# Kernel optimization log

Hardware: AMD Instinct MI355X
Metric: run time of the kernel (lower is better)

The kernel has to match this reference:

```python
import jax, jax.numpy as jnp
import numpy as np

B, T, D = 4, 4096, 1024
LN_EPS = 1e-5

def _xavier(key, shape, gain=1.0):
    fan_in, fan_out = shape[1], shape[0]
    a = gain * np.sqrt(6.0 / (fan_in + fan_out))
    return jax.random.uniform(key, shape, jnp.float32, -a, a)

def setup_inputs() -> dict:
    key = jax.random.key(0)
    kx, kg, kv, ko = jax.random.split(key, 4)
    # log_decay param init so that softplus(log_decay) == decay_init (0.01)
    log_decay = jnp.asarray(np.log(np.expm1(0.01)), jnp.float32)
    return {
        "x": jax.random.normal(kx, (B, T, D), jnp.float32),
        "ln_w": jnp.ones((D,), jnp.float32),
        "ln_b": jnp.zeros((D,), jnp.float32),
        "gate_w": _xavier(kg, (D, D)),            # torch Linear weight [out, in]
        "gate_b": jnp.zeros((D,), jnp.float32),
        "value_w": _xavier(kv, (D, D), gain=0.01),
        "value_b": jnp.zeros((D,), jnp.float32),
        "out_w": _xavier(ko, (D, D), gain=0.01),
        "out_b": jnp.zeros((D,), jnp.float32),
        "log_decay": log_decay,
    }

def reference(x, ln_w, ln_b, gate_w, gate_b, value_w, value_b, out_w, out_b, log_decay):
    # LayerNorm over last dim
    mu = jnp.mean(x, axis=-1, keepdims=True)
    var = jnp.mean(jnp.square(x - mu), axis=-1, keepdims=True)
    normed = (x - mu) * jax.lax.rsqrt(var + LN_EPS) * ln_w + ln_b
    # gate / value projections (torch Linear: y = x @ W.T + b)
    g = jax.nn.sigmoid(normed @ gate_w.T + gate_b)
    v = normed @ value_w.T + value_b
    # push-pull: cumsum(g*v) - cumsum((1-g)*v) == cumsum((2g-1)*v)
    cumsum = jnp.cumsum((2.0 * g - 1.0) * v, axis=1)
    alpha = jax.nn.softplus(log_decay)
    positions = jnp.arange(T, dtype=jnp.float32)
    decay = jnp.exp(-alpha * positions)[None, :, None]  # [1, T, 1]
    output = cumsum * decay
    return x + (output @ out_w.T + out_b)
```

## Files before the change

### kernel.cpp

```cpp
#include <hip/hip_runtime.h>
#include <hip/hip_bf16.h>

#define BB 4
#define TT 4096
#define DD 1024
#define MM (BB * TT)
#define LN_EPS 1e-5f

typedef __attribute__((ext_vector_type(8))) short bf16x8;
typedef __attribute__((ext_vector_type(4))) float f32x4;

__device__ __forceinline__ float bfbits2f(unsigned short h) {
    return __uint_as_float(((unsigned int)h) << 16);
}
__device__ __forceinline__ unsigned short f2bfbits(float f) {
    __hip_bfloat16 h = __float2bfloat16(f);
    return *reinterpret_cast<unsigned short*>(&h);
}
__device__ __forceinline__ unsigned int pack2(float a, float b) {
    return (unsigned int)f2bfbits(a) | ((unsigned int)f2bfbits(b) << 16);
}

__device__ __forceinline__ void async_copy16(void* lds, const void* g) {
    __builtin_amdgcn_global_load_lds(
        (const __attribute__((address_space(1))) void*)g,
        (__attribute__((address_space(3))) void*)lds,
        16, 0, 0);
}

__global__ __launch_bounds__(256)
void convert_w3(const float* __restrict__ s0, const float* __restrict__ s1,
                const float* __restrict__ s2,
                __hip_bfloat16* __restrict__ d0, __hip_bfloat16* __restrict__ d1,
                __hip_bfloat16* __restrict__ d2)
{
    const int blk = blockIdx.x;
    const int w = blk >> 10;
    const float* src = (w == 0) ? s0 : (w == 1) ? s1 : s2;
    __hip_bfloat16* dst = (w == 0) ? d0 : (w == 1) ? d1 : d2;
    const size_t i = ((size_t)(blk & 1023) * 256 + threadIdx.x) * 4;
    float4 v = *(const float4*)(src + i);
    uint2 o;
    o.x = pack2(v.x, v.y);
    o.y = pack2(v.z, v.w);
    *(uint2*)((unsigned short*)dst + i) = o;
}

__global__ __launch_bounds__(256)
void ln_kernel(const float* __restrict__ x,
               const float* __restrict__ w,
               const float* __restrict__ b,
               __hip_bfloat16* __restrict__ out)
{
    const int wv   = threadIdx.x >> 6;
    const int lane = threadIdx.x & 63;
    const int row  = blockIdx.x * 4 + wv;

    const float* xr = x + (size_t)row * DD + lane * 16;
    float4 v[4];
    #pragma unroll
    for (int i = 0; i < 4; ++i) v[i] = *(const float4*)(xr + i * 4);

    float s = 0.0f, ss = 0.0f;
    #pragma unroll
    for (int i = 0; i < 4; ++i) {
        s  += (v[i].x + v[i].y) + (v[i].z + v[i].w);
        ss += fmaf(v[i].x, v[i].x, fmaf(v[i].y, v[i].y,
              fmaf(v[i].z, v[i].z, v[i].w * v[i].w)));
    }
    #pragma unroll
    for (int o = 32; o > 0; o >>= 1) {
        s  += __shfl_down(s, o);
        ss += __shfl_down(ss, o);
    }
    s  = __shfl(s, 0);
    ss = __shfl(ss, 0);

    const float mu   = s * (1.0f / DD);
    const float var  = ss * (1.0f / DD) - mu * mu;
    const float rstd = rsqrtf(var + LN_EPS);

    unsigned int res[8];
    #pragma unroll
    for (int i = 0; i < 4; ++i) {
        float4 wr = *(const float4*)(w + lane * 16 + i * 4);
        float4 br = *(const float4*)(b + lane * 16 + i * 4);
        float o0 = (v[i].x - mu) * rstd * wr.x + br.x;
        float o1 = (v[i].y - mu) * rstd * wr.y + br.y;
        float o2 = (v[i].z - mu) * rstd * wr.z + br.z;
        float o3 = (v[i].w - mu) * rstd * wr.w + br.w;
        res[i * 2]     = pack2(o0, o1);
        res[i * 2 + 1] = pack2(o2, o3);
    }
    unsigned short* op = (unsigned short*)out + (size_t)row * DD + lane * 16;
    *(uint4*)op       = make_uint4(res[0], res[1], res[2], res[3]);
    *(uint4*)(op + 8) = make_uint4(res[4], res[5], res[6], res[7]);
}

__global__ __launch_bounds__(256, 2)
void dual_gemm_gate(const __hip_bfloat16* __restrict__ A,
                    const __hip_bfloat16* __restrict__ Wg,
                    const __hip_bfloat16* __restrict__ Wv,
                    const float* __restrict__ gb,
                    const float* __restrict__ vb,
                    __hip_bfloat16* __restrict__ U,
                    int M, int N, int K)
{
    constexpr int BK = 64;
    __shared__ short As[128 * BK];
    __shared__ short Bg[128 * BK];
    __shared__ short Bv[128 * BK];

    const int tid  = threadIdx.x;
    const int m0   = blockIdx.x * 128;
    const int n0   = blockIdx.y * 128;
    const int wave = tid >> 6;
    const int lane = tid & 63;
    const int wm   = (wave & 1) * 64;
    const int wn   = (wave >> 1) * 64;
    const int lrow = lane & 15;
    const int kgrp = lane >> 4;
    const int swz  = lrow & 7;

    f32x4 accg[4][4] = {};
    f32x4 accv[4][4] = {};

    const __hip_bfloat16* gA[4];
    const __hip_bfloat16* gG[4];
    const __hip_bfloat16* gV[4];
    #pragma unroll
    for (int r = 0; r < 4; ++r) {
        const int slot = r * 256 + tid;
        const int srow = slot >> 3;
        const int gcc  = (slot & 7) ^ (srow & 7);
        gA[r] = A  + (size_t)(m0 + srow) * K + gcc * 8;
        gG[r] = Wg + (size_t)(n0 + srow) * K + gcc * 8;
        gV[r] = Wv + (size_t)(n0 + srow) * K + gcc * 8;
    }

    for (int k0 = 0; k0 < K; k0 += BK) {
        #pragma unroll
        for (int r = 0; r < 4; ++r) {
            async_copy16(&As[(r * 256 + tid) * 8], gA[r] + k0);
            async_copy16(&Bg[(r * 256 + tid) * 8], gG[r] + k0);
            async_copy16(&Bv[(r * 256 + tid) * 8], gV[r] + k0);
        }
        __builtin_amdgcn_s_waitcnt(0);
        __syncthreads();

        #pragma unroll
        for (int ks = 0; ks < 2; ++ks) {
            const int co = ((ks * 4 + kgrp) ^ swz) * 8;
            bf16x8 af[4], bgf[4], bvf[4];
            #pragma unroll
            for (int i = 0; i < 4; ++i)
                af[i] = *(const bf16x8*)&As[(wm + i * 16 + lrow) * BK + co];
            #pragma unroll
            for (int j = 0; j < 4; ++j) {
                bgf[j] = *(const bf16x8*)&Bg[(wn + j * 16 + lrow) * BK + co];
                bvf[j] = *(const bf16x8*)&Bv[(wn + j * 16 + lrow) * BK + co];
            }
            #pragma unroll
            for (int i = 0; i < 4; ++i)
                #pragma unroll
                for (int j = 0; j < 4; ++j) {
                    accg[i][j] = __builtin_amdgcn_mfma_f32_16x16x32_bf16(
                        bgf[j], af[i], accg[i][j], 0, 0, 0);
                    accv[i][j] = __builtin_amdgcn_mfma_f32_16x16x32_bf16(
                        bvf[j], af[i], accv[i][j], 0, 0, 0);
                }
        }
        __syncthreads();
    }

    #pragma unroll
    for (int j = 0; j < 4; ++j) {
        const int nb = n0 + wn + j * 16 + kgrp * 4;
        const float4 gb4 = *(const float4*)(gb + nb);
        const float4 vb4 = *(const float4*)(vb + nb);
        #pragma unroll
        for (int i = 0; i < 4; ++i) {
            const int m = m0 + wm + i * 16 + lrow;
            const float g0 = accg[i][j][0] + gb4.x, v0 = accv[i][j][0] + vb4.x;
            const float g1 = accg[i][j][1] + gb4.y, v1 = accv[i][j][1] + vb4.y;
            const float g2 = accg[i][j][2] + gb4.z, v2 = accv[i][j][2] + vb4.z;
            const float g3 = accg[i][j][3] + gb4.w, v3 = accv[i][j][3] + vb4.w;
            const float u0 = (2.0f / (1.0f + __expf(-g0)) - 1.0f) * v0;
            const float u1 = (2.0f / (1.0f + __expf(-g1)) - 1.0f) * v1;
            const float u2 = (2.0f / (1.0f + __expf(-g2)) - 1.0f) * v2;
            const float u3 = (2.0f / (1.0f + __expf(-g3)) - 1.0f) * v3;
            uint2 o;
            o.x = pack2(u0, u1);
            o.y = pack2(u2, u3);
            *(uint2*)((unsigned short*)U + (size_t)m * N + nb) = o;
        }
    }
}

__global__ __launch_bounds__(256, 2)
void gemm_out(const __hip_bfloat16* __restrict__ A,
              const __hip_bfloat16* __restrict__ W,
              const float* __restrict__ bias,
              const float* __restrict__ X,
              float* __restrict__ C,
              int M, int N, int K)
{
    constexpr int BK = 64;
    __shared__ short As[128 * BK];
    __shared__ short Bs[128 * BK];

    const int tid  = threadIdx.x;
    const int m0   = blockIdx.x * 128;
    const int n0   = blockIdx.y * 128;
    const int wave = tid >> 6;
    const int lane = tid & 63;
    const int wm   = (wave & 1) * 64;
    const int wn   = (wave >> 1) * 64;
    const int lrow = lane & 15;
    const int kgrp = lane >> 4;
    const int swz  = lrow & 7;

    f32x4 acc[4][4] = {};

    const __hip_bfloat16* gA[4];
    const __hip_bfloat16* gB[4];
    #pragma unroll
    for (int r = 0; r < 4; ++r) {
        const int slot = r * 256 + tid;
        const int srow = slot >> 3;
        const int gcc  = (slot & 7) ^ (srow & 7);
        gA[r] = A + (size_t)(m0 + srow) * K + gcc * 8;
        gB[r] = W + (size_t)(n0 + srow) * K + gcc * 8;
    }

    for (int k0 = 0; k0 < K; k0 += BK) {
        #pragma unroll
        for (int r = 0; r < 4; ++r) {
            async_copy16(&As[(r * 256 + tid) * 8], gA[r] + k0);
            async_copy16(&Bs[(r * 256 + tid) * 8], gB[r] + k0);
        }
        __builtin_amdgcn_s_waitcnt(0);
        __syncthreads();

        #pragma unroll
        for (int ks = 0; ks < 2; ++ks) {
            const int co = ((ks * 4 + kgrp) ^ swz) * 8;
            bf16x8 af[4], bfr[4];
            #pragma unroll
            for (int i = 0; i < 4; ++i)
                af[i] = *(const bf16x8*)&As[(wm + i * 16 + lrow) * BK + co];
            #pragma unroll
            for (int j = 0; j < 4; ++j)
                bfr[j] = *(const bf16x8*)&Bs[(wn + j * 16 + lrow) * BK + co];
            #pragma unroll
            for (int i = 0; i < 4; ++i)
                #pragma unroll
                for (int j = 0; j < 4; ++j)
                    acc[i][j] = __builtin_amdgcn_mfma_f32_16x16x32_bf16(
                        bfr[j], af[i], acc[i][j], 0, 0, 0);
        }
        __syncthreads();
    }

    #pragma unroll
    for (int j = 0; j < 4; ++j) {
        const int nb = n0 + wn + j * 16 + kgrp * 4;
        const float4 bv = *(const float4*)(bias + nb);
        #pragma unroll
        for (int i = 0; i < 4; ++i) {
            const int m = m0 + wm + i * 16 + lrow;
            const size_t idx = (size_t)m * N + nb;
            const float4 xv = *(const float4*)(X + idx);
            float4 o;
            o.x = acc[i][j][0] + bv.x + xv.x;
            o.y = acc[i][j][1] + bv.y + xv.y;
            o.z = acc[i][j][2] + bv.z + xv.z;
            o.w = acc[i][j][3] + bv.w + xv.w;
            *(float4*)(C + idx) = o;
        }
    }
}

#define NC 64
#define CL 64

__global__ __launch_bounds__(128)
void scan_partial(const __hip_bfloat16* __restrict__ U, float* __restrict__ Pk)
{
    const int c = blockIdx.x, b = blockIdx.y;
    const int d8 = threadIdx.x * 8;
    const unsigned short* p = (const unsigned short*)U +
        ((size_t)b * TT + (size_t)c * CL) * DD + d8;
    float s[8] = {};
    #pragma unroll 8
    for (int t = 0; t < CL; ++t) {
        uint4 raw = *(const uint4*)(p + (size_t)t * DD);
        unsigned int wds[4] = {raw.x, raw.y, raw.z, raw.w};
        #pragma unroll
        for (int k = 0; k < 4; ++k) {
            s[2 * k]     += bfbits2f((unsigned short)(wds[k] & 0xFFFF));
            s[2 * k + 1] += bfbits2f((unsigned short)(wds[k] >> 16));
        }
    }
    float* o = &Pk[((size_t)b * NC + c) * DD + d8];
    *(float4*)o       = make_float4(s[0], s[1], s[2], s[3]);
    *(float4*)(o + 4) = make_float4(s[4], s[5], s[6], s[7]);
}

__global__ __launch_bounds__(256)
void scan_offsets(float* __restrict__ Pk)
{
    const int col4 = ((int)blockIdx.x * 256 + (int)threadIdx.x) * 4;
    const int b = col4 >> 10;
    const int d = col4 & 1023;
    float r0 = 0, r1 = 0, r2 = 0, r3 = 0;
    float* p = Pk + (size_t)b * NC * DD + d;
    #pragma unroll 8
    for (int c = 0; c < NC; ++c) {
        float4 v = *(float4*)(p + (size_t)c * DD);
        *(float4*)(p + (size_t)c * DD) = make_float4(r0, r1, r2, r3);
        r0 += v.x; r1 += v.y; r2 += v.z; r3 += v.w;
    }
}

__global__ __launch_bounds__(128)
void scan_final(const __hip_bfloat16* __restrict__ U,
                const float* __restrict__ Pk,
                const float* __restrict__ log_decay,
                __hip_bfloat16* __restrict__ S)
{
    const int c = blockIdx.x, b = blockIdx.y;
    const int d8 = threadIdx.x * 8;

    const float ld = log_decay[0];
    const float alpha = log1pf(__expf(ld));
    const float ratio = __expf(-alpha);
    float dec = __expf(-alpha * (float)(c * CL));

    const float* pk = &Pk[((size_t)b * NC + c) * DD + d8];
    float run[8];
    float4 r0 = *(const float4*)pk;
    float4 r1 = *(const float4*)(pk + 4);
    run[0] = r0.x; run[1] = r0.y; run[2] = r0.z; run[3] = r0.w;
    run[4] = r1.x; run[5] = r1.y; run[6] = r1.z; run[7] = r1.w;

    const size_t base = ((size_t)b * TT + (size_t)c * CL) * DD + d8;
    const unsigned short* up = (const unsigned short*)U + base;
    unsigned short* sp = (unsigned short*)S + base;

    #pragma unroll 8
    for (int t = 0; t < CL; ++t) {
        uint4 raw = *(const uint4*)(up + (size_t)t * DD);
        unsigned int wds[4] = {raw.x, raw.y, raw.z, raw.w};
        uint4 o;
        unsigned int* ow = (unsigned int*)&o;
        #pragma unroll
        for (int k = 0; k < 4; ++k) {
            run[2 * k]     += bfbits2f((unsigned short)(wds[k] & 0xFFFF));
            run[2 * k + 1] += bfbits2f((unsigned short)(wds[k] >> 16));
            ow[k] = pack2(run[2 * k] * dec, run[2 * k + 1] * dec);
        }
        *(uint4*)(sp + (size_t)t * DD) = o;
        dec *= ratio;
    }
}

extern "C" void kernel_launch(void* const* d_in, const int* in_sizes, int n_in,
                              void* d_out, int out_size, void* d_ws, size_t ws_size,
                              hipStream_t stream)
{
    const float* x        = (const float*)d_in[0];
    const float* ln_w     = (const float*)d_in[1];
    const float* ln_b     = (const float*)d_in[2];
    const float* gate_w   = (const float*)d_in[3];
    const float* gate_b   = (const float*)d_in[4];
    const float* value_w  = (const float*)d_in[5];
    const float* value_b  = (const float*)d_in[6];
    const float* out_w    = (const float*)d_in[7];
    const float* out_b    = (const float*)d_in[8];
    const float* log_dec  = (const float*)d_in[9];
    float* out = (float*)d_out;

    char* ws = (char*)d_ws;
    const size_t MB = 1024 * 1024;
    __hip_bfloat16* normed = (__hip_bfloat16*)(ws);
    __hip_bfloat16* S      = (__hip_bfloat16*)(ws);
    float*          Pk     = (float*)(ws + 32 * MB);
    __hip_bfloat16* Wg16   = (__hip_bfloat16*)(ws + 33 * MB);
    __hip_bfloat16* Wv16   = (__hip_bfloat16*)(ws + 35 * MB);
    __hip_bfloat16* Wo16   = (__hip_bfloat16*)(ws + 37 * MB);
    __hip_bfloat16* U      = (__hip_bfloat16*)d_out;

    convert_w3<<<dim3(3072), dim3(256), 0, stream>>>(
        gate_w, value_w, out_w, Wg16, Wv16, Wo16);

    ln_kernel<<<dim3(MM / 4), dim3(256), 0, stream>>>(x, ln_w, ln_b, normed);

    dual_gemm_gate<<<dim3(MM / 128, DD / 128), dim3(256), 0, stream>>>(
        normed, Wg16, Wv16, gate_b, value_b, U, MM, DD, DD);

    scan_partial<<<dim3(NC, BB), dim3(128), 0, stream>>>(U, Pk);
    scan_offsets<<<dim3(4), dim3(256), 0, stream>>>(Pk);
    scan_final<<<dim3(NC, BB), dim3(128), 0, stream>>>(U, Pk, log_dec, S);

    gemm_out<<<dim3(MM / 128, DD / 128), dim3(256), 0, stream>>>(
        S, Wo16, out_b, x, out, MM, DD, DD);
}
```

Measured before the change: 297.3 us.

## Fuse chunk partial sums into gate GEMM epilogue and parallelize scan offsets

The dual GEMM epilogue now reduces each 64-row chunk of u values across lanes with xor shuffles and writes the per-chunk column sums straight to Pk. This removes the separate scan_partial kernel, which re-read all of U from memory. The chunk-sums are taken on fp32 values before bf16 rounding, so they differ slightly from the old sums of rounded values. scan_offsets is also rewritten to run on 64 blocks, each doing an LDS-tiled segmented exclusive prefix over the chunks, instead of 4 blocks with one serial loop per thread.

```diff
diff --git a/kernel.cpp b/kernel.cpp
--- a/kernel.cpp
+++ b/kernel.cpp
@@ -6,6 +6,9 @@
 #define DD 1024
 #define MM (BB * TT)
 #define LN_EPS 1e-5f
+
+#define NC 64
+#define CL 64
 
 typedef __attribute__((ext_vector_type(8))) short bf16x8;
 typedef __attribute__((ext_vector_type(4))) float f32x4;
@@ -104,6 +107,7 @@
                     const float* __restrict__ gb,
                     const float* __restrict__ vb,
                     __hip_bfloat16* __restrict__ U,
+                    float* __restrict__ Pk,
                     int M, int N, int K)
 {
     constexpr int BK = 64;
@@ -173,11 +177,16 @@
         __syncthreads();
     }
 
+    const int chrow = m0 + wm;
+    const int cb    = chrow >> 12;
+    const int cc    = (chrow & (TT - 1)) >> 6;
+
     #pragma unroll
     for (int j = 0; j < 4; ++j) {
         const int nb = n0 + wn + j * 16 + kgrp * 4;
         const float4 gb4 = *(const float4*)(gb + nb);
         const float4 vb4 = *(const float4*)(vb + nb);
+        float4 ps = make_float4(0.f, 0.f, 0.f, 0.f);
         #pragma unroll
         for (int i = 0; i < 4; ++i) {
             const int m = m0 + wm + i * 16 + lrow;
@@ -189,11 +198,21 @@
             const float u1 = (2.0f / (1.0f + __expf(-g1)) - 1.0f) * v1;
             const float u2 = (2.0f / (1.0f + __expf(-g2)) - 1.0f) * v2;
             const float u3 = (2.0f / (1.0f + __expf(-g3)) - 1.0f) * v3;
+            ps.x += u0; ps.y += u1; ps.z += u2; ps.w += u3;
             uint2 o;
             o.x = pack2(u0, u1);
             o.y = pack2(u2, u3);
             *(uint2*)((unsigned short*)U + (size_t)m * N + nb) = o;
         }
+        #pragma unroll
+        for (int mk = 1; mk <= 8; mk <<= 1) {
+            ps.x += __shfl_xor(ps.x, mk);
+            ps.y += __shfl_xor(ps.y, mk);
+            ps.z += __shfl_xor(ps.z, mk);
+            ps.w += __shfl_xor(ps.w, mk);
+        }
+        if (lrow == 0)
+            *(float4*)&Pk[((size_t)cb * NC + cc) * DD + nb] = ps;
     }
 }
 
@@ -281,45 +300,50 @@
     }
 }
 
-#define NC 64
-#define CL 64
-
-__global__ __launch_bounds__(128)
-void scan_partial(const __hip_bfloat16* __restrict__ U, float* __restrict__ Pk)
-{
-    const int c = blockIdx.x, b = blockIdx.y;
-    const int d8 = threadIdx.x * 8;
-    const unsigned short* p = (const unsigned short*)U +
-        ((size_t)b * TT + (size_t)c * CL) * DD + d8;
-    float s[8] = {};
-    #pragma unroll 8
-    for (int t = 0; t < CL; ++t) {
-        uint4 raw = *(const uint4*)(p + (size_t)t * DD);
-        unsigned int wds[4] = {raw.x, raw.y, raw.z, raw.w};
-        #pragma unroll
-        for (int k = 0; k < 4; ++k) {
-            s[2 * k]     += bfbits2f((unsigned short)(wds[k] & 0xFFFF));
-            s[2 * k + 1] += bfbits2f((unsigned short)(wds[k] >> 16));
-        }
-    }
-    float* o = &Pk[((size_t)b * NC + c) * DD + d8];
-    *(float4*)o       = make_float4(s[0], s[1], s[2], s[3]);
-    *(float4*)(o + 4) = make_float4(s[4], s[5], s[6], s[7]);
-}
-
 __global__ __launch_bounds__(256)
 void scan_offsets(float* __restrict__ Pk)
 {
-    const int col4 = ((int)blockIdx.x * 256 + (int)threadIdx.x) * 4;
-    const int b = col4 >> 10;
-    const int d = col4 & 1023;
-    float r0 = 0, r1 = 0, r2 = 0, r3 = 0;
-    float* p = Pk + (size_t)b * NC * DD + d;
-    #pragma unroll 8
-    for (int c = 0; c < NC; ++c) {
-        float4 v = *(float4*)(p + (size_t)c * DD);
-        *(float4*)(p + (size_t)c * DD) = make_float4(r0, r1, r2, r3);
-        r0 += v.x; r1 += v.y; r2 += v.z; r3 += v.w;
+    __shared__ float Tl[64][68];
+    __shared__ float Seg[4][64];
+
+    const int tid  = threadIdx.x;
+    const int col0 = blockIdx.x * 64;
+    const int b    = col0 >> 10;
+    const int d0   = col0 & 1023;
+
+    #pragma unroll
+    for (int r = 0; r < 4; ++r) {
+        const int idx = r * 256 + tid;
+        const int c = idx >> 4, q = idx & 15;
+        float4 v = *(const float4*)&Pk[((size_t)b * NC + c) * DD + d0 + q * 4];
+        *(float4*)&Tl[c][q * 4] = v;
+    }
+    __syncthreads();
+
+    const int j = tid & 63, seg = tid >> 6;
+    float ssum = 0.0f;
+    #pragma unroll
+    for (int k = 0; k < 16; ++k) ssum += Tl[seg * 16 + k][j];
+    Seg[seg][j] = ssum;
+    __syncthreads();
+
+    float run = 0.0f;
+    for (int s = 0; s < seg; ++s) run += Seg[s][j];
+    #pragma unroll
+    for (int k = 0; k < 16; ++k) {
+        const int c = seg * 16 + k;
+        const float v = Tl[c][j];
+        Tl[c][j] = run;
+        run += v;
+    }
+    __syncthreads();
+
+    #pragma unroll
+    for (int r = 0; r < 4; ++r) {
+        const int idx = r * 256 + tid;
+        const int c = idx >> 4, q = idx & 15;
+        *(float4*)&Pk[((size_t)b * NC + c) * DD + d0 + q * 4] =
+            *(const float4*)&Tl[c][q * 4];
     }
 }
 
@@ -397,10 +421,9 @@
     ln_kernel<<<dim3(MM / 4), dim3(256), 0, stream>>>(x, ln_w, ln_b, normed);
 
     dual_gemm_gate<<<dim3(MM / 128, DD / 128), dim3(256), 0, stream>>>(
-        normed, Wg16, Wv16, gate_b, value_b, U, MM, DD, DD);
-
-    scan_partial<<<dim3(NC, BB), dim3(128), 0, stream>>>(U, Pk);
-    scan_offsets<<<dim3(4), dim3(256), 0, stream>>>(Pk);
+        normed, Wg16, Wv16, gate_b, value_b, U, Pk, MM, DD, DD);
+
+    scan_offsets<<<dim3(NC), dim3(256), 0, stream>>>(Pk);
     scan_final<<<dim3(NC, BB), dim3(128), 0, stream>>>(U, Pk, log_dec, S);
 
     gemm_out<<<dim3(MM / 128, DD / 128), dim3(256), 0, stream>>>(
```

New measurement: 292.8 us. Within noise of the previous version (-1.5%).
